# Kernel tuning notes

Measured on AMD Instinct MI355X. Metric: run time of the kernel, lower is better.

## Reference

```python
import jax, jax.numpy as jnp
import numpy as np

C = 1024
H = 64
W = 64


def _conv1x1(x, Wt, b):
    # x: [1, Cin, H, W], Wt: [Cout, Cin] -> [1, Cout, H, W]
    return jnp.einsum('oc,bchw->bohw', Wt, x) + b[None, :, None, None]


def setup_inputs() -> dict:
    key = jax.random.key(0)
    ks = jax.random.split(key, 12)
    sc = 1.0 / np.sqrt(C)
    return {
        'x_f': jax.random.normal(ks[0], (1, C, H, W), jnp.float32),
        'x_m': jax.random.normal(ks[1], (1, C, H, W), jnp.float32),
        'x_l': jax.random.normal(ks[2], (1, C, H, W), jnp.float32),
        'Wq': jax.random.normal(ks[3], (C // 2, C), jnp.float32) * sc,
        'bq': jax.random.normal(ks[4], (C // 2,), jnp.float32) * sc,
        'Wk1': jax.random.normal(ks[5], (C // 2, C), jnp.float32) * sc,
        'bk1': jax.random.normal(ks[6], (C // 2,), jnp.float32) * sc,
        'Wk2': jax.random.normal(ks[7], (C // 2, C), jnp.float32) * sc,
        'bk2': jax.random.normal(ks[8], (C // 2,), jnp.float32) * sc,
        'Wv': jax.random.normal(ks[9], (C, C), jnp.float32) * sc,
        'bv': jax.random.normal(ks[10], (C,), jnp.float32) * sc,
        'gamma': jax.random.normal(ks[11], (1,), jnp.float32),
    }


def reference(x_f, x_m, x_l, Wq, bq, Wk1, bk1, Wk2, bk2, Wv, bv, gamma):
    c = x_f.shape[1]
    h, w = x_f.shape[2], x_f.shape[3]
    # torch .view(1, C, -1) on a [1, C/2, H, W] tensor: row-major reshape to [C, H*W/2]
    q = _conv1x1(x_m, Wq, bq).reshape(c, -1).T      # [HW/2, C]
    kf = _conv1x1(x_f, Wk1, bk1).reshape(c, -1)     # [C, HW/2]
    kl = _conv1x1(x_l, Wk2, bk2).reshape(c, -1)     # [C, HW/2]
    att_f = jax.nn.softmax(kf @ q, axis=-1)         # [C, C]
    att_l = jax.nn.softmax(kl @ q, axis=-1)         # [C, C]
    v = _conv1x1(x_m, Wv, bv).reshape(c, -1)        # [C, HW]
    out = att_f @ v + att_l @ v                     # [C, HW]
    out = out.reshape(1, c, h, w)
    return gamma * out + (x_l + x_f) / 2
```

## Files before the change

kernel.cpp:

```cpp
#include <hip/hip_runtime.h>
#include <math.h>


typedef __attribute__((ext_vector_type(8))) short    bf16x8;
typedef __attribute__((ext_vector_type(4))) float    f32x4;

__device__ __forceinline__ unsigned short f2bf(float x) {
    unsigned u = __float_as_uint(x);
    u += 0x7FFFu + ((u >> 16) & 1u);
    return (unsigned short)(u >> 16);
}
__device__ __forceinline__ float bf2f(unsigned short h) {
    return __uint_as_float(((unsigned)h) << 16);
}
__device__ __forceinline__ void split2(float x, unsigned short& h, unsigned short& l) {
    h = f2bf(x);
    l = f2bf(x - bf2f(h));
}

__global__ __launch_bounds__(256) void split_plain_k(
    const float* __restrict__ X, unsigned short* __restrict__ H,
    unsigned short* __restrict__ L)
{
    const size_t i = ((size_t)blockIdx.x * 256 + threadIdx.x) * 4;
    const float4 v = *(const float4*)(X + i);
    ushort4 h, l;
    split2(v.x, h.x, l.x); split2(v.y, h.y, l.y);
    split2(v.z, h.z, l.z); split2(v.w, h.w, l.w);
    *(ushort4*)(H + i) = h;
    *(ushort4*)(L + i) = l;
}

__global__ __launch_bounds__(256) void transpose_split_k(
    const float* __restrict__ X, unsigned short* __restrict__ Th,
    unsigned short* __restrict__ Tl)
{
    __shared__ float t[32 * 33];
    const int tid = threadIdx.x;
    const int c0 = blockIdx.y * 32;
    const int p0 = blockIdx.x * 32;

    const int cl = tid >> 3;
    const int p4 = (tid & 7) * 4;
    const float4 v = *(const float4*)(X + (size_t)(c0 + cl) * 4096 + p0 + p4);
    t[(p4 + 0) * 33 + cl] = v.x;
    t[(p4 + 1) * 33 + cl] = v.y;
    t[(p4 + 2) * 33 + cl] = v.z;
    t[(p4 + 3) * 33 + cl] = v.w;
    __syncthreads();

    const int pl = tid >> 3;
    const int c4 = (tid & 7) * 4;
    ushort4 h, l;
    split2(t[pl * 33 + c4 + 0], h.x, l.x);
    split2(t[pl * 33 + c4 + 1], h.y, l.y);
    split2(t[pl * 33 + c4 + 2], h.z, l.z);
    split2(t[pl * 33 + c4 + 3], h.w, l.w);
    const size_t o = (size_t)(p0 + pl) * 1024 + c0 + c4;
    *(ushort4*)(Th + o) = h;
    *(ushort4*)(Tl + o) = l;
}

__global__ __launch_bounds__(256) void transpose_reduce_split_k(
    const float* __restrict__ P0, const float* __restrict__ P1,
    const float* __restrict__ bias,
    unsigned short* __restrict__ Th, unsigned short* __restrict__ Tl)
{
    __shared__ float t[32 * 33];
    const int tid = threadIdx.x;
    const int c0 = blockIdx.y * 32;
    const int p0 = blockIdx.x * 32;

    const int cl = tid >> 3;
    const int p4 = (tid & 7) * 4;
    const size_t g = (size_t)(c0 + cl) * 4096 + p0 + p4;
    const float4 v0 = *(const float4*)(P0 + g);
    const float4 v1 = *(const float4*)(P1 + g);
    const float b = bias[c0 + cl];
    t[(p4 + 0) * 33 + cl] = v0.x + v1.x + b;
    t[(p4 + 1) * 33 + cl] = v0.y + v1.y + b;
    t[(p4 + 2) * 33 + cl] = v0.z + v1.z + b;
    t[(p4 + 3) * 33 + cl] = v0.w + v1.w + b;
    __syncthreads();

    const int pl = tid >> 3;
    const int c4 = (tid & 7) * 4;
    ushort4 h, l;
    split2(t[pl * 33 + c4 + 0], h.x, l.x);
    split2(t[pl * 33 + c4 + 1], h.y, l.y);
    split2(t[pl * 33 + c4 + 2], h.z, l.z);
    split2(t[pl * 33 + c4 + 3], h.w, l.w);
    const size_t o = (size_t)(p0 + pl) * 1024 + c0 + c4;
    *(ushort4*)(Th + o) = h;
    *(ushort4*)(Tl + o) = l;
}

__device__ __forceinline__ void gemm_core(
    const unsigned short* __restrict__ Ah, const unsigned short* __restrict__ Al,
    const unsigned short* __restrict__ Bh, const unsigned short* __restrict__ Bl,
    int ldk, int kbeg, int kend, int m0, int n0,
    unsigned short* As_h, unsigned short* As_l,
    unsigned short* Bs_h, unsigned short* Bs_l,
    f32x4 (&acc)[4][4])
{
    const int tid  = threadIdx.x;
    const int lane = tid & 63;
    const int wv   = tid >> 6;
    const int wm   = (wv >> 1) * 64;
    const int wn   = (wv & 1) * 64;
    const int lr   = lane & 15;
    const int quad = lane >> 4;
    const int r0 = tid >> 2;
    const int sg = (tid & 3) * 8;

    for (int k0 = kbeg; k0 < kend; k0 += 32) {
        const size_t ka = (size_t)(m0 + r0) * ldk + k0 + sg;
        const size_t kb = (size_t)(n0 + r0) * ldk + k0 + sg;
        const bf16x8 a0h = *(const bf16x8*)(Ah + ka);
        const bf16x8 a1h = *(const bf16x8*)(Ah + ka + (size_t)64 * ldk);
        const bf16x8 a0l = *(const bf16x8*)(Al + ka);
        const bf16x8 a1l = *(const bf16x8*)(Al + ka + (size_t)64 * ldk);
        const bf16x8 b0h = *(const bf16x8*)(Bh + kb);
        const bf16x8 b1h = *(const bf16x8*)(Bh + kb + (size_t)64 * ldk);
        const bf16x8 b0l = *(const bf16x8*)(Bl + kb);
        const bf16x8 b1l = *(const bf16x8*)(Bl + kb + (size_t)64 * ldk);

        __syncthreads();
        *(bf16x8*)(As_h + r0 * 40 + sg)        = a0h;
        *(bf16x8*)(As_h + (r0 + 64) * 40 + sg) = a1h;
        *(bf16x8*)(As_l + r0 * 40 + sg)        = a0l;
        *(bf16x8*)(As_l + (r0 + 64) * 40 + sg) = a1l;
        *(bf16x8*)(Bs_h + r0 * 40 + sg)        = b0h;
        *(bf16x8*)(Bs_h + (r0 + 64) * 40 + sg) = b1h;
        *(bf16x8*)(Bs_l + r0 * 40 + sg)        = b0l;
        *(bf16x8*)(Bs_l + (r0 + 64) * 40 + sg) = b1l;
        __syncthreads();

        bf16x8 afh[4], afl[4], bfh[4], bfl[4];
#pragma unroll
        for (int i = 0; i < 4; ++i) {
            const int ra = (wm + i * 16 + lr) * 40 + quad * 8;
            afh[i] = *(const bf16x8*)(As_h + ra);
            afl[i] = *(const bf16x8*)(As_l + ra);
            const int rb = (wn + i * 16 + lr) * 40 + quad * 8;
            bfh[i] = *(const bf16x8*)(Bs_h + rb);
            bfl[i] = *(const bf16x8*)(Bs_l + rb);
        }
#pragma unroll
        for (int i = 0; i < 4; ++i)
#pragma unroll
            for (int j = 0; j < 4; ++j) {
                acc[i][j] = __builtin_amdgcn_mfma_f32_16x16x32_bf16(afh[i], bfh[j], acc[i][j], 0, 0, 0);
                acc[i][j] = __builtin_amdgcn_mfma_f32_16x16x32_bf16(afh[i], bfl[j], acc[i][j], 0, 0, 0);
                acc[i][j] = __builtin_amdgcn_mfma_f32_16x16x32_bf16(afl[i], bfh[j], acc[i][j], 0, 0, 0);
            }
    }
}

#define GEMM_PROLOGUE()                                                 \
    __shared__ unsigned short As_h[128 * 40], As_l[128 * 40];           \
    __shared__ unsigned short Bs_h[128 * 40], Bs_l[128 * 40];           \
    f32x4 acc[4][4];                                                    \
    _Pragma("unroll") for (int i = 0; i < 4; ++i)                       \
    _Pragma("unroll") for (int j = 0; j < 4; ++j)                       \
    _Pragma("unroll") for (int r = 0; r < 4; ++r) acc[i][j][r] = 0.f;   \
    const int lane = threadIdx.x & 63;                                  \
    const int wv   = threadIdx.x >> 6;                                  \
    const int wm   = (wv >> 1) * 64;                                    \
    const int wn   = (wv & 1) * 64;                                     \
    const int lr   = lane & 15;                                         \
    const int quad = lane >> 4;

__global__ __launch_bounds__(256) void conv_qk_fused_k(
    const unsigned short* __restrict__ Wqh, const unsigned short* __restrict__ Wql,
    const unsigned short* __restrict__ Wk1h, const unsigned short* __restrict__ Wk1l,
    const unsigned short* __restrict__ Wk2h, const unsigned short* __restrict__ Wk2l,
    const unsigned short* __restrict__ xmTh, const unsigned short* __restrict__ xmTl,
    const unsigned short* __restrict__ xfTh, const unsigned short* __restrict__ xfTl,
    const unsigned short* __restrict__ xlTh, const unsigned short* __restrict__ xlTl,
    const float* __restrict__ bq, const float* __restrict__ bk1,
    const float* __restrict__ bk2,
    unsigned short* __restrict__ Qh, unsigned short* __restrict__ Ql,
    unsigned short* __restrict__ Kfh, unsigned short* __restrict__ Kfl,
    unsigned short* __restrict__ Klh, unsigned short* __restrict__ Kll)
{
    GEMM_PROLOGUE();
    const int z = blockIdx.z;
    const unsigned short *Ah, *Al, *Bh, *Bl;
    const float* bias;
    unsigned short *Ch, *Cl;
    if (z == 0)      { Ah = Wqh;  Al = Wql;  Bh = xmTh; Bl = xmTl; bias = bq;  Ch = Qh;  Cl = Ql;  }
    else if (z == 1) { Ah = Wk1h; Al = Wk1l; Bh = xfTh; Bl = xfTl; bias = bk1; Ch = Kfh; Cl = Kfl; }
    else             { Ah = Wk2h; Al = Wk2l; Bh = xlTh; Bl = xlTl; bias = bk2; Ch = Klh; Cl = Kll; }
    const int m0 = blockIdx.y * 128;
    const int n0 = blockIdx.x * 128;

    gemm_core(Ah, Al, Bh, Bl, 1024, 0, 1024, m0, n0, As_h, As_l, Bs_h, Bs_l, acc);

#pragma unroll
    for (int i = 0; i < 4; ++i) {
        const int mb = m0 + wm + i * 16 + quad * 4;
#pragma unroll
        for (int j = 0; j < 4; ++j) {
            const int nn = n0 + wn + j * 16 + lr;
#pragma unroll
            for (int r = 0; r < 4; ++r) {
                const float v = acc[i][j][r] + bias[mb + r];
                const size_t idx = (size_t)(mb + r) * 4096 + nn;
                unsigned short h, l;
                split2(v, h, l);
                Ch[idx] = h;
                Cl[idx] = l;
            }
        }
    }
}

__global__ __launch_bounds__(256) void conv_v_split_k(
    const unsigned short* __restrict__ Wvh, const unsigned short* __restrict__ Wvl,
    const unsigned short* __restrict__ xmTh, const unsigned short* __restrict__ xmTl,
    float* __restrict__ Vp0, float* __restrict__ Vp1)
{
    GEMM_PROLOGUE();
    const int z = blockIdx.z;
    float* out = z ? Vp1 : Vp0;
    const int m0 = blockIdx.y * 128;
    const int n0 = blockIdx.x * 128;

    gemm_core(Wvh, Wvl, xmTh, xmTl, 1024, z * 512, z * 512 + 512, m0, n0,
              As_h, As_l, Bs_h, Bs_l, acc);

#pragma unroll
    for (int i = 0; i < 4; ++i) {
        const int mb = m0 + wm + i * 16 + quad * 4;
#pragma unroll
        for (int j = 0; j < 4; ++j) {
            const int nn = n0 + wn + j * 16 + lr;
#pragma unroll
            for (int r = 0; r < 4; ++r)
                out[(size_t)(mb + r) * 4096 + nn] = acc[i][j][r];
        }
    }
}

__global__ __launch_bounds__(256) void logits_fused_k(
    const unsigned short* __restrict__ Kfh, const unsigned short* __restrict__ Kfl,
    const unsigned short* __restrict__ Klh, const unsigned short* __restrict__ Kll,
    const unsigned short* __restrict__ Qh, const unsigned short* __restrict__ Ql,
    float* __restrict__ Sfp, float* __restrict__ Slp)
{
    GEMM_PROLOGUE();
    const int which = blockIdx.z >> 2;
    const int slice = blockIdx.z & 3;
    const unsigned short* Ah = which ? Klh : Kfh;
    const unsigned short* Al = which ? Kll : Kfl;
    float* out = (which ? Slp : Sfp) + (size_t)slice * 1024 * 1024;
    const int m0 = blockIdx.y * 128;
    const int n0 = blockIdx.x * 128;

    gemm_core(Ah, Al, Qh, Ql, 2048, slice * 512, slice * 512 + 512, m0, n0,
              As_h, As_l, Bs_h, Bs_l, acc);

#pragma unroll
    for (int i = 0; i < 4; ++i) {
        const int mb = m0 + wm + i * 16 + quad * 4;
#pragma unroll
        for (int j = 0; j < 4; ++j) {
            const int nn = n0 + wn + j * 16 + lr;
#pragma unroll
            for (int r = 0; r < 4; ++r)
                out[(size_t)(mb + r) * 1024 + nn] = acc[i][j][r];
        }
    }
}

__global__ __launch_bounds__(256) void gemm_final_k(
    const unsigned short* __restrict__ Amh, const unsigned short* __restrict__ Aml,
    const unsigned short* __restrict__ VTh, const unsigned short* __restrict__ VTl,
    float* __restrict__ out,
    const float* __restrict__ xf, const float* __restrict__ xl,
    const float* __restrict__ gamma)
{
    GEMM_PROLOGUE();
    const int m0 = blockIdx.y * 128;
    const int n0 = blockIdx.x * 128;

    gemm_core(Amh, Aml, VTh, VTl, 1024, 0, 1024, m0, n0,
              As_h, As_l, Bs_h, Bs_l, acc);

    const float g = gamma[0];
#pragma unroll
    for (int i = 0; i < 4; ++i) {
        const int mb = m0 + wm + i * 16 + quad * 4;
#pragma unroll
        for (int j = 0; j < 4; ++j) {
            const int nn = n0 + wn + j * 16 + lr;
#pragma unroll
            for (int r = 0; r < 4; ++r) {
                const size_t idx = (size_t)(mb + r) * 4096 + nn;
                out[idx] = g * acc[i][j][r] + 0.5f * (xf[idx] + xl[idx]);
            }
        }
    }
}

__global__ __launch_bounds__(256) void softmax_add4_k(
    const float* __restrict__ Sfp, const float* __restrict__ Slp,
    unsigned short* __restrict__ Ah, unsigned short* __restrict__ Al)
{
    const int row = blockIdx.x;
    const int tid = threadIdx.x;
    __shared__ float red[8];
    const size_t base = (size_t)row * 1024 + tid * 4;
    const size_t SL = (size_t)1024 * 1024;

    float4 vf = *(const float4*)(Sfp + base);
    float4 vl = *(const float4*)(Slp + base);
#pragma unroll
    for (int s = 1; s < 4; ++s) {
        const float4 a = *(const float4*)(Sfp + s * SL + base);
        const float4 b = *(const float4*)(Slp + s * SL + base);
        vf.x += a.x; vf.y += a.y; vf.z += a.z; vf.w += a.w;
        vl.x += b.x; vl.y += b.y; vl.z += b.z; vl.w += b.w;
    }

    float mf = fmaxf(fmaxf(vf.x, vf.y), fmaxf(vf.z, vf.w));
    float ml = fmaxf(fmaxf(vl.x, vl.y), fmaxf(vl.z, vl.w));
#pragma unroll
    for (int off = 32; off; off >>= 1) {
        mf = fmaxf(mf, __shfl_down(mf, off, 64));
        ml = fmaxf(ml, __shfl_down(ml, off, 64));
    }
    const int wave = tid >> 6;
    if ((tid & 63) == 0) { red[wave] = mf; red[4 + wave] = ml; }
    __syncthreads();
    mf = fmaxf(fmaxf(red[0], red[1]), fmaxf(red[2], red[3]));
    ml = fmaxf(fmaxf(red[4], red[5]), fmaxf(red[6], red[7]));
    __syncthreads();

    const float4 ef = make_float4(expf(vf.x - mf), expf(vf.y - mf),
                                  expf(vf.z - mf), expf(vf.w - mf));
    const float4 el = make_float4(expf(vl.x - ml), expf(vl.y - ml),
                                  expf(vl.z - ml), expf(vl.w - ml));
    float sf = ef.x + ef.y + ef.z + ef.w;
    float sl = el.x + el.y + el.z + el.w;
#pragma unroll
    for (int off = 32; off; off >>= 1) {
        sf += __shfl_down(sf, off, 64);
        sl += __shfl_down(sl, off, 64);
    }
    if ((tid & 63) == 0) { red[wave] = sf; red[4 + wave] = sl; }
    __syncthreads();
    sf = red[0] + red[1] + red[2] + red[3];
    sl = red[4] + red[5] + red[6] + red[7];

    const float rf = 1.f / sf, rl = 1.f / sl;
    ushort4 h, l;
    split2(ef.x * rf + el.x * rl, h.x, l.x);
    split2(ef.y * rf + el.y * rl, h.y, l.y);
    split2(ef.z * rf + el.z * rl, h.z, l.z);
    split2(ef.w * rf + el.w * rl, h.w, l.w);
    *(ushort4*)(Ah + base) = h;
    *(ushort4*)(Al + base) = l;
}

__global__ void noop_k(float* p) { if (threadIdx.x == 1024) p[0] = 0.f; }

extern "C" void kernel_launch(void* const* d_in, const int* in_sizes, int n_in,
                              void* d_out, int out_size, void* d_ws, size_t ws_size,
                              hipStream_t stream) {
    (void)in_sizes; (void)n_in; (void)out_size;
    const float* xf  = (const float*)d_in[0];
    const float* xm  = (const float*)d_in[1];
    const float* xl  = (const float*)d_in[2];
    const float* Wq  = (const float*)d_in[3];
    const float* bq  = (const float*)d_in[4];
    const float* Wk1 = (const float*)d_in[5];
    const float* bk1 = (const float*)d_in[6];
    const float* Wk2 = (const float*)d_in[7];
    const float* bk2 = (const float*)d_in[8];
    const float* Wv  = (const float*)d_in[9];
    const float* bv  = (const float*)d_in[10];
    const float* gamma = (const float*)d_in[11];
    float* out = (float*)d_out;

    const size_t MB = 1024 * 1024;
    if (ws_size < 98 * MB) {
        noop_k<<<dim3(1), dim3(64), 0, stream>>>((float*)d_ws);
        return;
    }

    char* p = (char*)d_ws;
    unsigned short* xmT_h = (unsigned short*)(p + 0 * MB);
    unsigned short* xmT_l = (unsigned short*)(p + 8 * MB);
    unsigned short* xfT_h = (unsigned short*)(p + 16 * MB);
    unsigned short* xfT_l = (unsigned short*)(p + 24 * MB);
    unsigned short* xlT_h = (unsigned short*)(p + 32 * MB);
    unsigned short* xlT_l = (unsigned short*)(p + 40 * MB);
    unsigned short* Wq_h  = (unsigned short*)(p + 48 * MB);
    unsigned short* Wq_l  = (unsigned short*)(p + 49 * MB);
    unsigned short* Wk1_h = (unsigned short*)(p + 50 * MB);
    unsigned short* Wk1_l = (unsigned short*)(p + 51 * MB);
    unsigned short* Wk2_h = (unsigned short*)(p + 52 * MB);
    unsigned short* Wk2_l = (unsigned short*)(p + 53 * MB);
    unsigned short* Wv_h  = (unsigned short*)(p + 54 * MB);
    unsigned short* Wv_l  = (unsigned short*)(p + 56 * MB);
    unsigned short* Q_h   = (unsigned short*)(p + 58 * MB);
    unsigned short* Q_l   = (unsigned short*)(p + 62 * MB);
    unsigned short* Kf_h  = (unsigned short*)(p + 66 * MB);
    unsigned short* Kf_l  = (unsigned short*)(p + 70 * MB);
    unsigned short* Kl_h  = (unsigned short*)(p + 74 * MB);
    unsigned short* Kl_l  = (unsigned short*)(p + 78 * MB);
    float*          Sfp  = (float*)(p + 16 * MB);
    float*          Slp  = (float*)(p + 32 * MB);
    float*          Vp0  = (float*)(p + 82 * MB);
    float*          Vp1  = (float*)(p + 58 * MB);
    unsigned short* VT_h = xmT_h;
    unsigned short* VT_l = xmT_l;
    unsigned short* Am_h = (unsigned short*)(p + 74 * MB);
    unsigned short* Am_l = (unsigned short*)(p + 76 * MB);

    const dim3 blk(256);
    transpose_split_k<<<dim3(128, 32), blk, 0, stream>>>(xm, xmT_h, xmT_l);
    transpose_split_k<<<dim3(128, 32), blk, 0, stream>>>(xf, xfT_h, xfT_l);
    transpose_split_k<<<dim3(128, 32), blk, 0, stream>>>(xl, xlT_h, xlT_l);
    split_plain_k<<<dim3(512), blk, 0, stream>>>(Wq,  Wq_h,  Wq_l);
    split_plain_k<<<dim3(512), blk, 0, stream>>>(Wk1, Wk1_h, Wk1_l);
    split_plain_k<<<dim3(512), blk, 0, stream>>>(Wk2, Wk2_h, Wk2_l);
    split_plain_k<<<dim3(1024), blk, 0, stream>>>(Wv, Wv_h, Wv_l);
    conv_qk_fused_k<<<dim3(32, 4, 3), blk, 0, stream>>>(
        Wq_h, Wq_l, Wk1_h, Wk1_l, Wk2_h, Wk2_l,
        xmT_h, xmT_l, xfT_h, xfT_l, xlT_h, xlT_l,
        bq, bk1, bk2, Q_h, Q_l, Kf_h, Kf_l, Kl_h, Kl_l);
    logits_fused_k<<<dim3(8, 8, 8), blk, 0, stream>>>(
        Kf_h, Kf_l, Kl_h, Kl_l, Q_h, Q_l, Sfp, Slp);
    conv_v_split_k<<<dim3(32, 8, 2), blk, 0, stream>>>(
        Wv_h, Wv_l, xmT_h, xmT_l, Vp0, Vp1);
    transpose_reduce_split_k<<<dim3(128, 32), blk, 0, stream>>>(
        Vp0, Vp1, bv, VT_h, VT_l);
    softmax_add4_k<<<dim3(1024), blk, 0, stream>>>(Sfp, Slp, Am_h, Am_l);
    gemm_final_k<<<dim3(32, 8), blk, 0, stream>>>(
        Am_h, Am_l, VT_h, VT_l, out, xf, xl, gamma);
}
```

Measured before the change: 314.2 us.

## Merge input/weight split launches and fold V conv into fused conv kernel

The three activation transposes become one 3D-grid launch, and the four weight splits become one launch. The V 1x1 conv now runs as extra M-tiles of the fused Q/K conv kernel over the full K range, with the bias added in-kernel. This drops the split-K partial buffers and the reduce step, so V is written once in fp32 and then transposed and split by a plain transpose kernel. The goal is fewer launches and less partial-sum traffic, at the cost of a longer full-K GEMM per V tile and a per-element branch in the epilogue.

```diff
diff --git a/kernel.cpp b/kernel.cpp
--- a/kernel.cpp
+++ b/kernel.cpp
@@ -18,12 +18,22 @@
     l = f2bf(x - bf2f(h));
 }
 
-__global__ __launch_bounds__(256) void split_plain_k(
-    const float* __restrict__ X, unsigned short* __restrict__ H,
-    unsigned short* __restrict__ L)
-{
-    const size_t i = ((size_t)blockIdx.x * 256 + threadIdx.x) * 4;
-    const float4 v = *(const float4*)(X + i);
+__global__ __launch_bounds__(256) void weights_split_k(
+    const float* __restrict__ Wq, const float* __restrict__ Wk1,
+    const float* __restrict__ Wk2, const float* __restrict__ Wv,
+    unsigned short* __restrict__ Wqh, unsigned short* __restrict__ Wql,
+    unsigned short* __restrict__ Wk1h, unsigned short* __restrict__ Wk1l,
+    unsigned short* __restrict__ Wk2h, unsigned short* __restrict__ Wk2l,
+    unsigned short* __restrict__ Wvh, unsigned short* __restrict__ Wvl)
+{
+    const int gi = blockIdx.x;
+    const float* src; unsigned short *H, *L; int base;
+    if (gi < 512)       { src = Wq;  H = Wqh;  L = Wql;  base = gi; }
+    else if (gi < 1024) { src = Wk1; H = Wk1h; L = Wk1l; base = gi - 512; }
+    else if (gi < 1536) { src = Wk2; H = Wk2h; L = Wk2l; base = gi - 1024; }
+    else                { src = Wv;  H = Wvh;  L = Wvl;  base = gi - 1536; }
+    const size_t i = (size_t)base * 1024 + threadIdx.x * 4;
+    const float4 v = *(const float4*)(src + i);
     ushort4 h, l;
     split2(v.x, h.x, l.x); split2(v.y, h.y, l.y);
     split2(v.z, h.z, l.z); split2(v.w, h.w, l.w);
@@ -31,10 +41,18 @@
     *(ushort4*)(L + i) = l;
 }
 
-__global__ __launch_bounds__(256) void transpose_split_k(
-    const float* __restrict__ X, unsigned short* __restrict__ Th,
-    unsigned short* __restrict__ Tl)
-{
+__global__ __launch_bounds__(256) void transpose3_k(
+    const float* __restrict__ x0, const float* __restrict__ x1,
+    const float* __restrict__ x2,
+    unsigned short* __restrict__ t0h, unsigned short* __restrict__ t0l,
+    unsigned short* __restrict__ t1h, unsigned short* __restrict__ t1l,
+    unsigned short* __restrict__ t2h, unsigned short* __restrict__ t2l)
+{
+    const float* X; unsigned short *Th, *Tl;
+    if (blockIdx.z == 0)      { X = x0; Th = t0h; Tl = t0l; }
+    else if (blockIdx.z == 1) { X = x1; Th = t1h; Tl = t1l; }
+    else                      { X = x2; Th = t2h; Tl = t2l; }
+
     __shared__ float t[32 * 33];
     const int tid = threadIdx.x;
     const int c0 = blockIdx.y * 32;
@@ -61,9 +79,8 @@
     *(ushort4*)(Tl + o) = l;
 }
 
-__global__ __launch_bounds__(256) void transpose_reduce_split_k(
-    const float* __restrict__ P0, const float* __restrict__ P1,
-    const float* __restrict__ bias,
+__global__ __launch_bounds__(256) void transpose1_k(
+    const float* __restrict__ X,
     unsigned short* __restrict__ Th, unsigned short* __restrict__ Tl)
 {
     __shared__ float t[32 * 33];
@@ -73,14 +90,11 @@
 
     const int cl = tid >> 3;
     const int p4 = (tid & 7) * 4;
-    const size_t g = (size_t)(c0 + cl) * 4096 + p0 + p4;
-    const float4 v0 = *(const float4*)(P0 + g);
-    const float4 v1 = *(const float4*)(P1 + g);
-    const float b = bias[c0 + cl];
-    t[(p4 + 0) * 33 + cl] = v0.x + v1.x + b;
-    t[(p4 + 1) * 33 + cl] = v0.y + v1.y + b;
-    t[(p4 + 2) * 33 + cl] = v0.z + v1.z + b;
-    t[(p4 + 3) * 33 + cl] = v0.w + v1.w + b;
+    const float4 v = *(const float4*)(X + (size_t)(c0 + cl) * 4096 + p0 + p4);
+    t[(p4 + 0) * 33 + cl] = v.x;
+    t[(p4 + 1) * 33 + cl] = v.y;
+    t[(p4 + 2) * 33 + cl] = v.z;
+    t[(p4 + 3) * 33 + cl] = v.w;
     __syncthreads();
 
     const int pl = tid >> 3;
@@ -171,35 +185,48 @@
     const int lr   = lane & 15;                                         \
     const int quad = lane >> 4;
 
-__global__ __launch_bounds__(256) void conv_qk_fused_k(
+__global__ __launch_bounds__(256) void conv_all_k(
     const unsigned short* __restrict__ Wqh, const unsigned short* __restrict__ Wql,
     const unsigned short* __restrict__ Wk1h, const unsigned short* __restrict__ Wk1l,
     const unsigned short* __restrict__ Wk2h, const unsigned short* __restrict__ Wk2l,
+    const unsigned short* __restrict__ Wvh, const unsigned short* __restrict__ Wvl,
     const unsigned short* __restrict__ xmTh, const unsigned short* __restrict__ xmTl,
     const unsigned short* __restrict__ xfTh, const unsigned short* __restrict__ xfTl,
     const unsigned short* __restrict__ xlTh, const unsigned short* __restrict__ xlTl,
     const float* __restrict__ bq, const float* __restrict__ bk1,
-    const float* __restrict__ bk2,
+    const float* __restrict__ bk2, const float* __restrict__ bv,
     unsigned short* __restrict__ Qh, unsigned short* __restrict__ Ql,
     unsigned short* __restrict__ Kfh, unsigned short* __restrict__ Kfl,
-    unsigned short* __restrict__ Klh, unsigned short* __restrict__ Kll)
+    unsigned short* __restrict__ Klh, unsigned short* __restrict__ Kll,
+    float* __restrict__ V)
 {
     GEMM_PROLOGUE();
-    const int z = blockIdx.z;
+    const int mt = blockIdx.y;
     const unsigned short *Ah, *Al, *Bh, *Bl;
     const float* bias;
-    unsigned short *Ch, *Cl;
-    if (z == 0)      { Ah = Wqh;  Al = Wql;  Bh = xmTh; Bl = xmTl; bias = bq;  Ch = Qh;  Cl = Ql;  }
-    else if (z == 1) { Ah = Wk1h; Al = Wk1l; Bh = xfTh; Bl = xfTl; bias = bk1; Ch = Kfh; Cl = Kfl; }
-    else             { Ah = Wk2h; Al = Wk2l; Bh = xlTh; Bl = xlTl; bias = bk2; Ch = Klh; Cl = Kll; }
-    const int m0 = blockIdx.y * 128;
+    unsigned short *Ch = nullptr, *Cl = nullptr;
+    float* Cv = nullptr;
+    int mloc;
+    if (mt < 4) {
+        Ah = Wqh;  Al = Wql;  Bh = xmTh; Bl = xmTl; bias = bq;
+        Ch = Qh;   Cl = Ql;   mloc = mt * 128;
+    } else if (mt < 8) {
+        Ah = Wk1h; Al = Wk1l; Bh = xfTh; Bl = xfTl; bias = bk1;
+        Ch = Kfh;  Cl = Kfl;  mloc = (mt - 4) * 128;
+    } else if (mt < 12) {
+        Ah = Wk2h; Al = Wk2l; Bh = xlTh; Bl = xlTl; bias = bk2;
+        Ch = Klh;  Cl = Kll;  mloc = (mt - 8) * 128;
+    } else {
+        Ah = Wvh;  Al = Wvl;  Bh = xmTh; Bl = xmTl; bias = bv;
+        Cv = V;    mloc = (mt - 12) * 128;
+    }
     const int n0 = blockIdx.x * 128;
 
-    gemm_core(Ah, Al, Bh, Bl, 1024, 0, 1024, m0, n0, As_h, As_l, Bs_h, Bs_l, acc);
+    gemm_core(Ah, Al, Bh, Bl, 1024, 0, 1024, mloc, n0, As_h, As_l, Bs_h, Bs_l, acc);
 
 #pragma unroll
     for (int i = 0; i < 4; ++i) {
-        const int mb = m0 + wm + i * 16 + quad * 4;
+        const int mb = mloc + wm + i * 16 + quad * 4;
 #pragma unroll
         for (int j = 0; j < 4; ++j) {
             const int nn = n0 + wn + j * 16 + lr;
@@ -207,38 +234,15 @@
             for (int r = 0; r < 4; ++r) {
                 const float v = acc[i][j][r] + bias[mb + r];
                 const size_t idx = (size_t)(mb + r) * 4096 + nn;
-                unsigned short h, l;
-                split2(v, h, l);
-                Ch[idx] = h;
-                Cl[idx] = l;
+                if (Cv) {
+                    Cv[idx] = v;
+                } else {
+                    unsigned short h, l;
+                    split2(v, h, l);
+                    Ch[idx] = h;
+                    Cl[idx] = l;
+                }
             }
-        }
-    }
-}
-
-__global__ __launch_bounds__(256) void conv_v_split_k(
-    const unsigned short* __restrict__ Wvh, const unsigned short* __restrict__ Wvl,
-    const unsigned short* __restrict__ xmTh, const unsigned short* __restrict__ xmTl,
-    float* __restrict__ Vp0, float* __restrict__ Vp1)
-{
-    GEMM_PROLOGUE();
-    const int z = blockIdx.z;
-    float* out = z ? Vp1 : Vp0;
-    const int m0 = blockIdx.y * 128;
-    const int n0 = blockIdx.x * 128;
-
-    gemm_core(Wvh, Wvl, xmTh, xmTl, 1024, z * 512, z * 512 + 512, m0, n0,
-              As_h, As_l, Bs_h, Bs_l, acc);
-
-#pragma unroll
-    for (int i = 0; i < 4; ++i) {
-        const int mb = m0 + wm + i * 16 + quad * 4;
-#pragma unroll
-        for (int j = 0; j < 4; ++j) {
-            const int nn = n0 + wn + j * 16 + lr;
-#pragma unroll
-            for (int r = 0; r < 4; ++r)
-                out[(size_t)(mb + r) * 4096 + nn] = acc[i][j][r];
         }
     }
 }
@@ -411,33 +415,27 @@
     unsigned short* Kf_l  = (unsigned short*)(p + 70 * MB);
     unsigned short* Kl_h  = (unsigned short*)(p + 74 * MB);
     unsigned short* Kl_l  = (unsigned short*)(p + 78 * MB);
+    float*          V     = (float*)(p + 82 * MB);
     float*          Sfp  = (float*)(p + 16 * MB);
     float*          Slp  = (float*)(p + 32 * MB);
-    float*          Vp0  = (float*)(p + 82 * MB);
-    float*          Vp1  = (float*)(p + 58 * MB);
     unsigned short* VT_h = xmT_h;
     unsigned short* VT_l = xmT_l;
     unsigned short* Am_h = (unsigned short*)(p + 74 * MB);
     unsigned short* Am_l = (unsigned short*)(p + 76 * MB);
 
     const dim3 blk(256);
-    transpose_split_k<<<dim3(128, 32), blk, 0, stream>>>(xm, xmT_h, xmT_l);
-    transpose_split_k<<<dim3(128, 32), blk, 0, stream>>>(xf, xfT_h, xfT_l);
-    transpose_split_k<<<dim3(128, 32), blk, 0, stream>>>(xl, xlT_h, xlT_l);
-    split_plain_k<<<dim3(512), blk, 0, stream>>>(Wq,  Wq_h,  Wq_l);
-    split_plain_k<<<dim3(512), blk, 0, stream>>>(Wk1, Wk1_h, Wk1_l);
-    split_plain_k<<<dim3(512), blk, 0, stream>>>(Wk2, Wk2_h, Wk2_l);
-    split_plain_k<<<dim3(1024), blk, 0, stream>>>(Wv, Wv_h, Wv_l);
-    conv_qk_fused_k<<<dim3(32, 4, 3), blk, 0, stream>>>(
-        Wq_h, Wq_l, Wk1_h, Wk1_l, Wk2_h, Wk2_l,
+    transpose3_k<<<dim3(128, 32, 3), blk, 0, stream>>>(
+        xm, xf, xl, xmT_h, xmT_l, xfT_h, xfT_l, xlT_h, xlT_l);
+    weights_split_k<<<dim3(2560), blk, 0, stream>>>(
+        Wq, Wk1, Wk2, Wv, Wq_h, Wq_l, Wk1_h, Wk1_l, Wk2_h, Wk2_l, Wv_h, Wv_l);
+    conv_all_k<<<dim3(32, 20), blk, 0, stream>>>(
+        Wq_h, Wq_l, Wk1_h, Wk1_l, Wk2_h, Wk2_l, Wv_h, Wv_l,
         xmT_h, xmT_l, xfT_h, xfT_l, xlT_h, xlT_l,
-        bq, bk1, bk2, Q_h, Q_l, Kf_h, Kf_l, Kl_h, Kl_l);
+        bq, bk1, bk2, bv,
+        Q_h, Q_l, Kf_h, Kf_l, Kl_h, Kl_l, V);
     logits_fused_k<<<dim3(8, 8, 8), blk, 0, stream>>>(
         Kf_h, Kf_l, Kl_h, Kl_l, Q_h, Q_l, Sfp, Slp);
-    conv_v_split_k<<<dim3(32, 8, 2), blk, 0, stream>>>(
-        Wv_h, Wv_l, xmT_h, xmT_l, Vp0, Vp1);
-    transpose_reduce_split_k<<<dim3(128, 32), blk, 0, stream>>>(
-        Vp0, Vp1, bv, VT_h, VT_l);
+    transpose1_k<<<dim3(128, 32), blk, 0, stream>>>(V, VT_h, VT_l);
     softmax_add4_k<<<dim3(1024), blk, 0, stream>>>(Sfp, Slp, Am_h, Am_l);
     gemm_final_k<<<dim3(32, 8), blk, 0, stream>>>(
         Am_h, Am_l, VT_h, VT_l, out, xf, xl, gamma);
```

After: 310.7 us. No clear change (-1.1%).
